# Optimization experiments

Hardware: AMD Instinct MI355X
Metric: run time of the kernel (lower is better)

The kernel has to match this reference:

```python
import jax, jax.numpy as jnp
import numpy as np

VAR_NUM = 96
EMBED_TIME = 128
INPUT_DIM = VAR_NUM * 2 + EMBED_TIME  # 320
ATTN_DIM = 64
N_HEADS = 8
ALL_DIM = ATTN_DIM * N_HEADS  # 512
B, N = 8, 2048
NEG_INF = -1e9  # finite stand-in for masked_fill(-inf); safe under softmax


def setup_inputs() -> dict:
    key = jax.random.key(0)
    ks = jax.random.split(key, 16)
    s = lambda d: 1.0 / np.sqrt(d)
    return {
        "times_in": jax.random.uniform(ks[0], (B, N), jnp.float32),
        "data_in": jax.random.normal(ks[1], (B, N, VAR_NUM), jnp.float32),
        "mask_in": jnp.ones((B, N, VAR_NUM), jnp.float32),
        "exist_times": jax.random.randint(ks[2], (B, N), 0, 2, jnp.int32),
        # TimeEmbedding params
        "w_per": jax.random.normal(ks[3], (1, EMBED_TIME - 1), jnp.float32),
        "b_per": jnp.zeros((EMBED_TIME - 1,), jnp.float32),
        "w_lin": jax.random.normal(ks[4], (1, 1), jnp.float32),
        "b_lin": jnp.zeros((1,), jnp.float32),
        # Attention params
        "Wq": jax.random.normal(ks[5], (INPUT_DIM, ALL_DIM), jnp.float32) * s(INPUT_DIM),
        "bq": jnp.zeros((ALL_DIM,), jnp.float32),
        "Wk": jax.random.normal(ks[6], (INPUT_DIM, ALL_DIM), jnp.float32) * s(INPUT_DIM),
        "bk": jnp.zeros((ALL_DIM,), jnp.float32),
        "Wv": jax.random.normal(ks[7], (INPUT_DIM, ALL_DIM), jnp.float32) * s(INPUT_DIM),
        "bv": jnp.zeros((ALL_DIM,), jnp.float32),
        "Wfc": jax.random.normal(ks[8], (ALL_DIM, ATTN_DIM), jnp.float32) * s(ALL_DIM),
        "bfc": jnp.zeros((ATTN_DIM,), jnp.float32),
    }


def reference(times_in, data_in, mask_in, exist_times,
              w_per, b_per, w_lin, b_lin,
              Wq, bq, Wk, bk, Wv, bv, Wfc, bfc):
    b, n = times_in.shape
    tt = times_in[..., None]  # [b, n, 1]
    # TimeEmbedding: [linear(tt), sin(periodic(tt))]
    te = jnp.concatenate([tt @ w_lin + b_lin, jnp.sin(tt @ w_per + b_per)], axis=-1)
    x = jnp.concatenate([data_in, mask_in, te], axis=-1)  # [b, n, INPUT_DIM]

    def heads(w, bias):
        return (x @ w + bias).reshape(b, n, N_HEADS, ATTN_DIM).transpose(0, 2, 1, 3)

    q, k, v = heads(Wq, bq), heads(Wk, bk), heads(Wv, bv)  # [b, h, n, d]
    # NOTE: custom scale uses sqrt(input_dim), not sqrt(head_dim)
    scores = jnp.einsum("bhqd,bhkd->bhqk", q, k) / jnp.sqrt(jnp.float32(INPUT_DIM))
    m = (exist_times != 0)
    scores = jnp.where(m[:, None, None, :], scores, NEG_INF)  # mask keys
    attn = jax.nn.softmax(scores, axis=-1)  # dropout p=0 in eval reference
    out = jnp.einsum("bhqk,bhkd->bhqd", attn, v)
    out = jnp.where(m[:, None, :, None], out, 0.0)  # zero masked query rows
    out = out.transpose(0, 2, 1, 3).reshape(b, n, ALL_DIM)
    return out @ Wfc + bfc  # [b, n, ATTN_DIM]
```

## Files before the change

kernel.cpp:

```cpp
#include <hip/hip_runtime.h>

#define N_ 2048
#define BN 16384
#define IN_DIM 320
#define QKV_N 1536
#define ALPHA 0.08064911f

typedef float f32x4 __attribute__((ext_vector_type(4)));
typedef short v8s __attribute__((ext_vector_type(8)));
typedef unsigned int u32x2 __attribute__((ext_vector_type(2)));

__device__ __forceinline__ short f2b(float f) {
  unsigned u = __builtin_bit_cast(unsigned, f);
  u = u + 0x7fff + ((u >> 16) & 1);
  return (short)(u >> 16);
}

__device__ __forceinline__ int piperm(int t) {
  return ((t >> 5) & 1) * 32 + ((t >> 2) & 3) * 8 + ((t >> 4) & 1) * 4 + (t & 3);
}

__global__ void build_x(const float* __restrict__ times, const float* __restrict__ data,
                        const float* __restrict__ maskv, const float* __restrict__ w_per,
                        const float* __restrict__ b_per, const float* __restrict__ w_lin,
                        const float* __restrict__ b_lin, const int* __restrict__ exist,
                        short* __restrict__ x, short* __restrict__ flagsg) {
  int row = blockIdx.x;
  int t = threadIdx.x;
  float tt = times[row];
  short* xr = x + (size_t)row * IN_DIM;
  const float* dr = data + (size_t)row * 96;
  const float* mr = maskv + (size_t)row * 96;
  if (t < 96) { xr[t] = f2b(dr[t]); xr[96 + t] = f2b(mr[t]); }
  float val;
  if (t == 0) {
    val = tt * w_lin[0] + b_lin[0];
    flagsg[(row & ~63) | piperm(row & 63)] = (exist[row] != 0) ? (short)0x3F80 : (short)0;
  } else {
    val = __sinf(tt * w_per[t - 1] + b_per[t - 1]);
  }
  xr[192 + t] = f2b(val);
}

__global__ void transpose_w(const float* __restrict__ Wq, const float* __restrict__ Wk,
                            const float* __restrict__ Wv, const float* __restrict__ Wfc,
                            short* __restrict__ Wt, short* __restrict__ WfcT) {
  int idx = blockIdx.x * 256 + threadIdx.x;
  if (idx < QKV_N * IN_DIM) {
    int n = idx / IN_DIM, kk = idx - n * IN_DIM;
    const float* W = (n < 512) ? Wq : (n < 1024 ? Wk : Wv);
    Wt[idx] = f2b(W[(size_t)kk * 512 + (n & 511)]);
  } else {
    int j = idx - QKV_N * IN_DIM;
    int d = j >> 9, kk = j & 511;
    WfcT[j] = f2b(Wfc[kk * 64 + d]);
  }
}

__launch_bounds__(256)
__global__ void qkv_gemm(const short* __restrict__ x, const short* __restrict__ Wt,
                         const float* __restrict__ bq, const float* __restrict__ bk,
                         const float* __restrict__ bv, const int* __restrict__ exist,
                         short* __restrict__ q, short* __restrict__ kT, short* __restrict__ vT) {
  __shared__ short As[128][40];
  __shared__ short Bs[128][40];
  int bm = blockIdx.x;
  int bn = blockIdx.y;
  int tid = threadIdx.x, wave = tid >> 6, lane = tid & 63;
  int wm = wave >> 1, wn = wave & 1;
  int l16 = lane & 15, lh = lane >> 4;
  f32x4 acc[4][4] = {};
  for (int kt = 0; kt < 10; ++kt) {
    int k0 = kt * 32;
#pragma unroll
    for (int s = 0; s < 2; ++s) {
      int c = tid + s * 256;
      int r = c >> 2, c8 = c & 3;
      *(v8s*)&As[r][c8 * 8] = *(const v8s*)&x[(size_t)(bm * 128 + r) * IN_DIM + k0 + c8 * 8];
      *(v8s*)&Bs[r][c8 * 8] = *(const v8s*)&Wt[(size_t)(bn * 128 + r) * IN_DIM + k0 + c8 * 8];
    }
    __syncthreads();
    v8s af[4], bfr[4];
#pragma unroll
    for (int m = 0; m < 4; ++m) af[m] = *(const v8s*)&As[wm * 64 + m * 16 + l16][lh * 8];
#pragma unroll
    for (int n = 0; n < 4; ++n) bfr[n] = *(const v8s*)&Bs[wn * 64 + n * 16 + l16][lh * 8];
#pragma unroll
    for (int m = 0; m < 4; ++m)
#pragma unroll
      for (int n = 0; n < 4; ++n)
        acc[m][n] = __builtin_amdgcn_mfma_f32_16x16x32_bf16(af[m], bfr[n], acc[m][n], 0, 0, 0);
    __syncthreads();
  }
  int w = bn >> 2;
  if (w == 0) {
#pragma unroll
    for (int m = 0; m < 4; ++m) {
      int row0 = bm * 128 + wm * 64 + m * 16 + lh * 4;
#pragma unroll
      for (int n = 0; n < 4; ++n) {
        int c = (bn * 128 + wn * 64 + n * 16 + l16) & 511;
        float bb = bq[c];
        int h = c >> 6, d = c & 63;
#pragma unroll
        for (int r = 0; r < 4; ++r) {
          int rr = row0 + r;
          int b = rr >> 11, ntok = rr & 2047;
          q[(((size_t)(b * 8 + h) * N_ + ntok) << 6) + d] = f2b((acc[m][n][r] + bb) * ALPHA);
        }
      }
    }
  } else if (w == 1) {
    int ktile = (bm * 2 + wm) & 31;
    int b = bm >> 4;
#pragma unroll
    for (int m = 0; m < 4; ++m) {
#pragma unroll
      for (int n = 0; n < 4; ++n) {
        int c = (bn * 128 + wn * 64 + n * 16 + l16) & 511;
        float bb = bk[c];
        int h = c >> 6;
        int d = n * 16 + l16;
        int kc2 = d >> 5, lh2 = (d >> 3) & 3, j = d & 7;
        size_t base = (((((size_t)((b * 8 + h) * 32 + ktile)) * 4 + m) * 2 + kc2) * 4 + lh2) * 128 + j;
#pragma unroll
        for (int r = 0; r < 4; ++r)
          kT[base + (lh * 4 + r) * 8] = f2b(acc[m][n][r] + bb);
      }
    }
  } else {
    int ktile = (bm * 2 + wm) & 31;
    int b = bm >> 4;
#pragma unroll
    for (int m = 0; m < 4; ++m) {
      int row0 = bm * 128 + wm * 64 + m * 16 + lh * 4;
      float fl[4];
#pragma unroll
      for (int r = 0; r < 4; ++r) fl[r] = (exist[row0 + r] != 0) ? 1.f : 0.f;
#pragma unroll
      for (int n = 0; n < 4; ++n) {
        int c = (bn * 128 + wn * 64 + n * 16 + l16) & 511;
        float bb = bv[c];
        int h = c >> 6;
        float v0 = (acc[m][n][0] + bb) * fl[0];
        float v1 = (acc[m][n][1] + bb) * fl[1];
        float v2 = (acc[m][n][2] + bb) * fl[2];
        float v3 = (acc[m][n][3] + bb) * fl[3];
        uint lopk, hipk;
        asm("v_cvt_pk_bf16_f32 %0, %1, %2" : "=v"(lopk) : "v"(v0), "v"(v1));
        asm("v_cvt_pk_bf16_f32 %0, %1, %2" : "=v"(hipk) : "v"(v2), "v"(v3));
        u32x2 pk2 = {lopk, hipk};
        size_t base = (((((size_t)((b * 8 + h) * 32 + ktile)) * 4 + n) * 2 + (m >> 1)) * 4 + lh) * 128
                      + l16 * 8 + (m & 1) * 4;
        *(u32x2*)&vT[base] = pk2;
      }
    }
  }
}

__launch_bounds__(256, 2)
__global__ void attn_kernel(const short* __restrict__ q, const short* __restrict__ kT,
                            const short* __restrict__ vT, const short* __restrict__ flagsg,
                            const int* __restrict__ exist, short* __restrict__ att) {
  int bx = blockIdx.x;
  int bh = ((bx >> 6) << 3) | (bx & 7);
  int qblk = (bx >> 3) & 7;
  int b = bh >> 3, h = bh & 7;
  int tid = threadIdx.x, wave = tid >> 6, lane = tid & 63;
  int l16 = lane & 15, lh = lane >> 4;
  int q0 = qblk * 256 + wave * 64;
  const short* qp = q + (size_t)bh * N_ * 64;
  const short* kpt = kT + (size_t)bh * 131072;
  const short* vpt = vT + (size_t)bh * 131072;
  const short* fpt = flagsg + b * N_;
  const int* ex = exist + b * N_;
  v8s qf[4][2];
#pragma unroll
  for (int m = 0; m < 4; ++m)
#pragma unroll
    for (int kc = 0; kc < 2; ++kc)
      qf[m][kc] = *(const v8s*)&qp[(size_t)(q0 + m * 16 + l16) * 64 + kc * 32 + lh * 8];
  f32x4 oacc[4][4] = {};
  f32x4 lacc[4] = {};
  const f32x4 zf = {0.f, 0.f, 0.f, 0.f};
  int voff = lane * 8;
  v8s kf[8], vf[8], ff[2];
#pragma unroll
  for (int i = 0; i < 8; ++i) {
    kf[i] = *(const v8s*)&kpt[i * 512 + voff];
    vf[i] = *(const v8s*)&vpt[i * 512 + voff];
  }
  ff[0] = *(const v8s*)&fpt[lh * 8];
  ff[1] = *(const v8s*)&fpt[32 + lh * 8];
#pragma unroll 1
  for (int kt = 0; kt < 32; ++kt) {
    const short* kn = kpt + (size_t)(kt + 1) * 4096;
    const short* vn = vpt + (size_t)(kt + 1) * 4096;
    const short* fn = fpt + (kt + 1) * 64;
#pragma unroll
    for (int mh = 0; mh < 2; ++mh) {
      f32x4 sacc[2][4];
#pragma unroll
      for (int n = 0; n < 4; ++n)
#pragma unroll
        for (int mm = 0; mm < 2; ++mm) {
          sacc[mm][n] = __builtin_amdgcn_mfma_f32_16x16x32_bf16(kf[n * 2], qf[mh * 2 + mm][0], zf, 0, 0, 0);
          sacc[mm][n] = __builtin_amdgcn_mfma_f32_16x16x32_bf16(kf[n * 2 + 1], qf[mh * 2 + mm][1], sacc[mm][n], 0, 0, 0);
        }
      if (mh == 1)
#pragma unroll
        for (int i = 0; i < 8; ++i) kf[i] = *(const v8s*)&kn[i * 512 + voff];
      v8s pf[2][2];
#pragma unroll
      for (int mm = 0; mm < 2; ++mm)
#pragma unroll
        for (int kc = 0; kc < 2; ++kc)
#pragma unroll
          for (int half = 0; half < 2; ++half) {
            int n = kc * 2 + half;
            float p0 = __builtin_amdgcn_exp2f(sacc[mm][n][0]);
            float p1 = __builtin_amdgcn_exp2f(sacc[mm][n][1]);
            float p2 = __builtin_amdgcn_exp2f(sacc[mm][n][2]);
            float p3 = __builtin_amdgcn_exp2f(sacc[mm][n][3]);
            uint w0, w1;
            asm("v_cvt_pk_bf16_f32 %0, %1, %2" : "=v"(w0) : "v"(p0), "v"(p1));
            asm("v_cvt_pk_bf16_f32 %0, %1, %2" : "=v"(w1) : "v"(p2), "v"(p3));
            ((uint*)&pf[mm][kc])[half * 2]     = w0;
            ((uint*)&pf[mm][kc])[half * 2 + 1] = w1;
          }
#pragma unroll
      for (int kc = 0; kc < 2; ++kc) {
#pragma unroll
        for (int mm = 0; mm < 2; ++mm)
          lacc[mh * 2 + mm] = __builtin_amdgcn_mfma_f32_16x16x32_bf16(pf[mm][kc], ff[kc], lacc[mh * 2 + mm], 0, 0, 0);
#pragma unroll
        for (int n = 0; n < 4; ++n)
#pragma unroll
          for (int mm = 0; mm < 2; ++mm)
            oacc[mh * 2 + mm][n] = __builtin_amdgcn_mfma_f32_16x16x32_bf16(pf[mm][kc], vf[n * 2 + kc], oacc[mh * 2 + mm][n], 0, 0, 0);
      }
    }
#pragma unroll
    for (int i = 0; i < 8; ++i) vf[i] = *(const v8s*)&vn[i * 512 + voff];
    ff[0] = *(const v8s*)&fn[lh * 8];
    ff[1] = *(const v8s*)&fn[32 + lh * 8];
  }
#pragma unroll
  for (int m = 0; m < 4; ++m)
#pragma unroll
    for (int r = 0; r < 4; ++r) {
      int row = q0 + m * 16 + lh * 4 + r;
      float qm = (ex[row] != 0) ? 1.f : 0.f;
      float inv = qm / fmaxf(lacc[m][r], 1e-20f);
#pragma unroll
      for (int n = 0; n < 4; ++n)
        att[((size_t)(b * N_ + row)) * 512 + h * 64 + n * 16 + l16] = f2b(oacc[m][n][r] * inv);
    }
}

__launch_bounds__(256)
__global__ void out_gemm(const short* __restrict__ att, const short* __restrict__ WfcT,
                         const float* __restrict__ bfc, float* __restrict__ out) {
  __shared__ short As[128][40];
  __shared__ short Bs[64][40];
  int bm = blockIdx.x;
  int tid = threadIdx.x, wave = tid >> 6, lane = tid & 63;
  int l16 = lane & 15, lh = lane >> 4;
  f32x4 acc[2][4] = {};
  for (int kt = 0; kt < 16; ++kt) {
    int k0 = kt * 32;
#pragma unroll
    for (int s = 0; s < 2; ++s) {
      int c = tid + s * 256;
      int r = c >> 2, c8 = c & 3;
      *(v8s*)&As[r][c8 * 8] = *(const v8s*)&att[(size_t)(bm * 128 + r) * 512 + k0 + c8 * 8];
    }
    { int r = tid >> 2, c8 = tid & 3;
      if (r < 64) *(v8s*)&Bs[r][c8 * 8] = *(const v8s*)&WfcT[(size_t)r * 512 + k0 + c8 * 8]; }
    __syncthreads();
    v8s bfr[4];
#pragma unroll
    for (int n = 0; n < 4; ++n) bfr[n] = *(const v8s*)&Bs[n * 16 + l16][lh * 8];
#pragma unroll
    for (int m = 0; m < 2; ++m) {
      v8s af = *(const v8s*)&As[wave * 32 + m * 16 + l16][lh * 8];
#pragma unroll
      for (int n = 0; n < 4; ++n)
        acc[m][n] = __builtin_amdgcn_mfma_f32_16x16x32_bf16(af, bfr[n], acc[m][n], 0, 0, 0);
    }
    __syncthreads();
  }
#pragma unroll
  for (int m = 0; m < 2; ++m)
#pragma unroll
    for (int n = 0; n < 4; ++n) {
      float bb = bfc[n * 16 + l16];
#pragma unroll
      for (int r = 0; r < 4; ++r) {
        int row = bm * 128 + wave * 32 + m * 16 + lh * 4 + r;
        out[(size_t)row * 64 + n * 16 + l16] = acc[m][n][r] + bb;
      }
    }
}

extern "C" void kernel_launch(void* const* d_in, const int* in_sizes, int n_in,
                              void* d_out, int out_size, void* d_ws, size_t ws_size,
                              hipStream_t stream) {
  const float* times = (const float*)d_in[0];
  const float* data  = (const float*)d_in[1];
  const float* maskv = (const float*)d_in[2];
  const int*   exist = (const int*)d_in[3];
  const float* w_per = (const float*)d_in[4];
  const float* b_per = (const float*)d_in[5];
  const float* w_lin = (const float*)d_in[6];
  const float* b_lin = (const float*)d_in[7];
  const float* Wq  = (const float*)d_in[8];
  const float* bq  = (const float*)d_in[9];
  const float* Wk  = (const float*)d_in[10];
  const float* bk  = (const float*)d_in[11];
  const float* Wv  = (const float*)d_in[12];
  const float* bv  = (const float*)d_in[13];
  const float* Wfc = (const float*)d_in[14];
  const float* bfc = (const float*)d_in[15];
  float* out = (float*)d_out;

  char* ws = (char*)d_ws;
  short* x     = (short*)(ws);
  short* Wt    = (short*)(ws + 10485760);
  short* WfcT  = (short*)(ws + 11468800);
  short* qb    = (short*)(ws + 11534336);
  short* kTb   = (short*)(ws + 28311552);
  short* vTb   = (short*)(ws + 45088768);
  short* att   = (short*)(ws + 61865984);
  short* flagsg= (short*)(ws + 78643200);

  build_x<<<BN, 128, 0, stream>>>(times, data, maskv, w_per, b_per, w_lin, b_lin, exist, x, flagsg);
  transpose_w<<<2048, 256, 0, stream>>>(Wq, Wk, Wv, Wfc, Wt, WfcT);
  qkv_gemm<<<dim3(128, 12), 256, 0, stream>>>(x, Wt, bq, bk, bv, exist, qb, kTb, vTb);
  attn_kernel<<<512, 256, 0, stream>>>(qb, kTb, vTb, flagsg, exist, att);
  out_gemm<<<128, 256, 0, stream>>>(att, WfcT, bfc, out);
}
```

Before: 125.1 us.

## Compact existing keys via prefix scan and skip masked key tiles in attention

Adds a per-batch prefix scan over the key existence mask so the QKV GEMM scatters only existing K/V rows into contiguous compacted tiles. The attention loop then iterates over only the non-empty key tiles, with flags marking valid slots in the last partial tile, which was zeroed beforehand. This removes roughly half the attention work for the random 0/1 mask, at the cost of scattered scalar K/V stores and two extra small kernels. Skipping masked keys is exact, since they contribute exp(-1e9)=0 in the reference.

```diff
diff --git a/kernel.cpp b/kernel.cpp
--- a/kernel.cpp
+++ b/kernel.cpp
@@ -23,8 +23,7 @@
 __global__ void build_x(const float* __restrict__ times, const float* __restrict__ data,
                         const float* __restrict__ maskv, const float* __restrict__ w_per,
                         const float* __restrict__ b_per, const float* __restrict__ w_lin,
-                        const float* __restrict__ b_lin, const int* __restrict__ exist,
-                        short* __restrict__ x, short* __restrict__ flagsg) {
+                        const float* __restrict__ b_lin, short* __restrict__ x) {
   int row = blockIdx.x;
   int t = threadIdx.x;
   float tt = times[row];
@@ -33,13 +32,52 @@
   const float* mr = maskv + (size_t)row * 96;
   if (t < 96) { xr[t] = f2b(dr[t]); xr[96 + t] = f2b(mr[t]); }
   float val;
-  if (t == 0) {
-    val = tt * w_lin[0] + b_lin[0];
-    flagsg[(row & ~63) | piperm(row & 63)] = (exist[row] != 0) ? (short)0x3F80 : (short)0;
-  } else {
-    val = __sinf(tt * w_per[t - 1] + b_per[t - 1]);
-  }
+  if (t == 0) val = tt * w_lin[0] + b_lin[0];
+  else        val = __sinf(tt * w_per[t - 1] + b_per[t - 1]);
   xr[192 + t] = f2b(val);
+}
+
+__global__ void scan_mask(const int* __restrict__ exist, int* __restrict__ prefix,
+                          int* __restrict__ ntg, short* __restrict__ flagsc) {
+  __shared__ int sums[256];
+  int b = blockIdx.x;
+  int t = threadIdx.x;
+  const int* e = exist + b * 2048;
+  int loc[8];
+  int s = 0;
+#pragma unroll
+  for (int j = 0; j < 8; ++j) { loc[j] = s; s += (e[t * 8 + j] != 0) ? 1 : 0; }
+  sums[t] = s;
+  __syncthreads();
+  for (int d = 1; d < 256; d <<= 1) {
+    int v = (t >= d) ? sums[t - d] : 0;
+    __syncthreads();
+    sums[t] += v;
+    __syncthreads();
+  }
+  int total = sums[255];
+  int base = (t == 0) ? 0 : sums[t - 1];
+#pragma unroll
+  for (int j = 0; j < 8; ++j) prefix[b * 2048 + t * 8 + j] = base + loc[j];
+  if (t == 0) ntg[b] = (total + 63) >> 6;
+#pragma unroll
+  for (int j = 0; j < 8; ++j) {
+    int slot = t * 8 + j;
+    flagsc[b * 2048 + (slot & ~63) + piperm(slot & 63)] =
+        (slot < total) ? (short)0x3F80 : (short)0;
+  }
+}
+
+__global__ void zero_pad(const int* __restrict__ ntg, short* __restrict__ kT,
+                         short* __restrict__ vT) {
+  int bh = blockIdx.x;
+  int nt = ntg[bh >> 3];
+  if (nt == 0) return;
+  size_t base = (size_t)bh * 131072 + (size_t)(nt - 1) * 4096;
+  int t = threadIdx.x;
+  v8s z = {0, 0, 0, 0, 0, 0, 0, 0};
+  *(v8s*)&kT[base + t * 8] = z;
+  *(v8s*)&vT[base + t * 8] = z;
 }
 
 __global__ void transpose_w(const float* __restrict__ Wq, const float* __restrict__ Wk,
@@ -61,6 +99,7 @@
 __global__ void qkv_gemm(const short* __restrict__ x, const short* __restrict__ Wt,
                          const float* __restrict__ bq, const float* __restrict__ bk,
                          const float* __restrict__ bv, const int* __restrict__ exist,
+                         const int* __restrict__ prefix,
                          short* __restrict__ q, short* __restrict__ kT, short* __restrict__ vT) {
   __shared__ short As[128][40];
   __shared__ short Bs[128][40];
@@ -111,10 +150,13 @@
       }
     }
   } else if (w == 1) {
-    int ktile = (bm * 2 + wm) & 31;
     int b = bm >> 4;
 #pragma unroll
     for (int m = 0; m < 4; ++m) {
+      int row0 = bm * 128 + wm * 64 + m * 16 + lh * 4;
+      int exr[4], dstr[4];
+#pragma unroll
+      for (int r = 0; r < 4; ++r) { exr[r] = exist[row0 + r]; dstr[r] = prefix[row0 + r]; }
 #pragma unroll
       for (int n = 0; n < 4; ++n) {
         int c = (bn * 128 + wn * 64 + n * 16 + l16) & 511;
@@ -122,37 +164,45 @@
         int h = c >> 6;
         int d = n * 16 + l16;
         int kc2 = d >> 5, lh2 = (d >> 3) & 3, j = d & 7;
-        size_t base = (((((size_t)((b * 8 + h) * 32 + ktile)) * 4 + m) * 2 + kc2) * 4 + lh2) * 128 + j;
-#pragma unroll
-        for (int r = 0; r < 4; ++r)
-          kT[base + (lh * 4 + r) * 8] = f2b(acc[m][n][r] + bb);
+        size_t hb = (size_t)(b * 8 + h) * 131072;
+#pragma unroll
+        for (int r = 0; r < 4; ++r) {
+          if (exr[r]) {
+            int dst = dstr[r];
+            size_t addr = hb + (size_t)(dst >> 6) * 4096
+                        + (size_t)((((dst >> 4) & 3) * 2 + kc2) * 512)
+                        + lh2 * 128 + (dst & 15) * 8 + j;
+            kT[addr] = f2b(acc[m][n][r] + bb);
+          }
+        }
       }
     }
   } else {
-    int ktile = (bm * 2 + wm) & 31;
     int b = bm >> 4;
 #pragma unroll
     for (int m = 0; m < 4; ++m) {
       int row0 = bm * 128 + wm * 64 + m * 16 + lh * 4;
-      float fl[4];
-#pragma unroll
-      for (int r = 0; r < 4; ++r) fl[r] = (exist[row0 + r] != 0) ? 1.f : 0.f;
+      int exr[4], dstr[4];
+#pragma unroll
+      for (int r = 0; r < 4; ++r) { exr[r] = exist[row0 + r]; dstr[r] = prefix[row0 + r]; }
 #pragma unroll
       for (int n = 0; n < 4; ++n) {
         int c = (bn * 128 + wn * 64 + n * 16 + l16) & 511;
         float bb = bv[c];
         int h = c >> 6;
-        float v0 = (acc[m][n][0] + bb) * fl[0];
-        float v1 = (acc[m][n][1] + bb) * fl[1];
-        float v2 = (acc[m][n][2] + bb) * fl[2];
-        float v3 = (acc[m][n][3] + bb) * fl[3];
-        uint lopk, hipk;
-        asm("v_cvt_pk_bf16_f32 %0, %1, %2" : "=v"(lopk) : "v"(v0), "v"(v1));
-        asm("v_cvt_pk_bf16_f32 %0, %1, %2" : "=v"(hipk) : "v"(v2), "v"(v3));
-        u32x2 pk2 = {lopk, hipk};
-        size_t base = (((((size_t)((b * 8 + h) * 32 + ktile)) * 4 + n) * 2 + (m >> 1)) * 4 + lh) * 128
-                      + l16 * 8 + (m & 1) * 4;
-        *(u32x2*)&vT[base] = pk2;
+        size_t hb = (size_t)(b * 8 + h) * 131072;
+#pragma unroll
+        for (int r = 0; r < 4; ++r) {
+          if (exr[r]) {
+            int dst = dstr[r];
+            int t2 = dst & 63;
+            int jj = ((t2 >> 4) & 1) * 4 + (t2 & 3);
+            size_t addr = hb + (size_t)(dst >> 6) * 4096
+                        + (size_t)((n * 2 + ((t2 >> 5) & 1)) * 512)
+                        + ((t2 >> 2) & 3) * 128 + l16 * 8 + jj;
+            vT[addr] = f2b(acc[m][n][r] + bb);
+          }
+        }
       }
     }
   }
@@ -160,8 +210,9 @@
 
 __launch_bounds__(256, 2)
 __global__ void attn_kernel(const short* __restrict__ q, const short* __restrict__ kT,
-                            const short* __restrict__ vT, const short* __restrict__ flagsg,
-                            const int* __restrict__ exist, short* __restrict__ att) {
+                            const short* __restrict__ vT, const short* __restrict__ flagsc,
+                            const int* __restrict__ ntg, const int* __restrict__ exist,
+                            short* __restrict__ att) {
   int bx = blockIdx.x;
   int bh = ((bx >> 6) << 3) | (bx & 7);
   int qblk = (bx >> 3) & 7;
@@ -169,10 +220,11 @@
   int tid = threadIdx.x, wave = tid >> 6, lane = tid & 63;
   int l16 = lane & 15, lh = lane >> 4;
   int q0 = qblk * 256 + wave * 64;
+  int nt = ntg[b];
   const short* qp = q + (size_t)bh * N_ * 64;
   const short* kpt = kT + (size_t)bh * 131072;
   const short* vpt = vT + (size_t)bh * 131072;
-  const short* fpt = flagsg + b * N_;
+  const short* fpt = flagsc + b * N_;
   const int* ex = exist + b * N_;
   v8s qf[4][2];
 #pragma unroll
@@ -193,10 +245,11 @@
   ff[0] = *(const v8s*)&fpt[lh * 8];
   ff[1] = *(const v8s*)&fpt[32 + lh * 8];
 #pragma unroll 1
-  for (int kt = 0; kt < 32; ++kt) {
+  for (int kt = 0; kt < nt; ++kt) {
     const short* kn = kpt + (size_t)(kt + 1) * 4096;
     const short* vn = vpt + (size_t)(kt + 1) * 4096;
     const short* fn = fpt + (kt + 1) * 64;
+    bool pre = (kt + 1 < nt);
 #pragma unroll
     for (int mh = 0; mh < 2; ++mh) {
       f32x4 sacc[2][4];
@@ -207,7 +260,7 @@
           sacc[mm][n] = __builtin_amdgcn_mfma_f32_16x16x32_bf16(kf[n * 2], qf[mh * 2 + mm][0], zf, 0, 0, 0);
           sacc[mm][n] = __builtin_amdgcn_mfma_f32_16x16x32_bf16(kf[n * 2 + 1], qf[mh * 2 + mm][1], sacc[mm][n], 0, 0, 0);
         }
-      if (mh == 1)
+      if (mh == 1 && pre)
 #pragma unroll
         for (int i = 0; i < 8; ++i) kf[i] = *(const v8s*)&kn[i * 512 + voff];
       v8s pf[2][2];
@@ -240,10 +293,12 @@
             oacc[mh * 2 + mm][n] = __builtin_amdgcn_mfma_f32_16x16x32_bf16(pf[mm][kc], vf[n * 2 + kc], oacc[mh * 2 + mm][n], 0, 0, 0);
       }
     }
-#pragma unroll
-    for (int i = 0; i < 8; ++i) vf[i] = *(const v8s*)&vn[i * 512 + voff];
-    ff[0] = *(const v8s*)&fn[lh * 8];
-    ff[1] = *(const v8s*)&fn[32 + lh * 8];
+    if (pre) {
+#pragma unroll
+      for (int i = 0; i < 8; ++i) vf[i] = *(const v8s*)&vn[i * 512 + voff];
+      ff[0] = *(const v8s*)&fn[lh * 8];
+      ff[1] = *(const v8s*)&fn[32 + lh * 8];
+    }
   }
 #pragma unroll
   for (int m = 0; m < 4; ++m)
@@ -332,11 +387,15 @@
   short* kTb   = (short*)(ws + 28311552);
   short* vTb   = (short*)(ws + 45088768);
   short* att   = (short*)(ws + 61865984);
-  short* flagsg= (short*)(ws + 78643200);
-
-  build_x<<<BN, 128, 0, stream>>>(times, data, maskv, w_per, b_per, w_lin, b_lin, exist, x, flagsg);
+  short* flagsc= (short*)(ws + 78643200);
+  int*   prefix= (int*)(ws + 78675968);
+  int*   ntg   = (int*)(ws + 78741504);
+
+  build_x<<<BN, 128, 0, stream>>>(times, data, maskv, w_per, b_per, w_lin, b_lin, x);
+  scan_mask<<<8, 256, 0, stream>>>(exist, prefix, ntg, flagsc);
+  zero_pad<<<64, 512, 0, stream>>>(ntg, kTb, vTb);
   transpose_w<<<2048, 256, 0, stream>>>(Wq, Wk, Wv, Wfc, Wt, WfcT);
-  qkv_gemm<<<dim3(128, 12), 256, 0, stream>>>(x, Wt, bq, bk, bv, exist, qb, kTb, vTb);
-  attn_kernel<<<512, 256, 0, stream>>>(qb, kTb, vTb, flagsg, exist, att);
+  qkv_gemm<<<dim3(128, 12), 256, 0, stream>>>(x, Wt, bq, bk, bv, exist, prefix, qb, kTb, vTb);
+  attn_kernel<<<512, 256, 0, stream>>>(qb, kTb, vTb, flagsc, ntg, exist, att);
   out_gemm<<<128, 256, 0, stream>>>(att, WfcT, bfc, out);
 }
```

After: 109.9 us. -12.1%, faster.
